# Optimization experiments

Hardware: AMD Instinct MI355X
Metric: run time of the kernel (lower is better)

Reference implementation:

```python
import jax, jax.numpy as jnp
import numpy as np

D_MODEL = 1024
N_HEADS = 16
D_HEAD = D_MODEL // N_HEADS
B, T = 4, 2048


def setup_inputs() -> dict:
    key = jax.random.key(0)
    k1, k2, k3 = jax.random.split(key, 3)
    x = jax.random.normal(k1, (B, T, D_MODEL), dtype=jnp.float32)
    # torch nn.Linear(d, 3d, bias=False): y = x @ W.T; here we store W.T directly.
    w_qkv = jax.random.normal(k2, (D_MODEL, 3 * D_MODEL), dtype=jnp.float32) * (1.0 / np.sqrt(D_MODEL))
    w_proj = jax.random.normal(k3, (D_MODEL, D_MODEL), dtype=jnp.float32) * (1.0 / np.sqrt(D_MODEL))
    return {"x": x, "w_qkv": w_qkv, "w_proj": w_proj}


def reference(x, w_qkv, w_proj):
    b, t, _ = x.shape
    qkv = x @ w_qkv  # [B, T, 3*D]
    q, k, v = jnp.split(qkv, 3, axis=-1)

    def split_heads(u):
        return u.reshape(b, t, N_HEADS, D_HEAD).transpose(0, 2, 1, 3)  # [B,H,T,Dh]

    q, k, v = split_heads(q), split_heads(k), split_heads(v)
    scale = 1.0 / np.sqrt(D_HEAD).astype(np.float32)
    scores = jnp.einsum('bhqd,bhkd->bhqk', q, k) * scale  # [B,H,T,T]
    attn = jax.nn.softmax(scores, axis=-1)
    out = jnp.einsum('bhqk,bhkd->bhqd', attn, v)  # [B,H,T,Dh]
    out = out.transpose(0, 2, 1, 3).reshape(b, t, D_MODEL)
    return out @ w_proj
```

## Files before the change

### kernel.cpp

```cpp
#include <hip/hip_runtime.h>
#include <hip/hip_bf16.h>
#include <stdint.h>

using bf16 = __bf16;
using bf16x8 = __attribute__((ext_vector_type(8))) __bf16;
using f32x4  = __attribute__((ext_vector_type(4))) float;
using f32x16 = __attribute__((ext_vector_type(16))) float;
using u32x4  = __attribute__((ext_vector_type(4))) uint32_t;

#define LOG2E 1.44269504088896340736f

constexpr int Tt = 2048;
constexpr int Dm = 1024;
constexpr int NH = 16;
constexpr int DH = 64;

__device__ inline void gll16(const void* g, void* l) {
  __builtin_amdgcn_global_load_lds((const __attribute__((address_space(1))) uint32_t*)g,
                                   (__attribute__((address_space(3))) uint32_t*)l, 16, 0, 0);
}

__device__ inline uint32_t cvtpk(float a, float b) {
  uint32_t r;
  asm("v_cvt_pk_bf16_f32 %0, %1, %2" : "=v"(r) : "v"(a), "v"(b));
  return r;
}
__device__ inline void pl32swap(uint32_t& a, uint32_t& b) {
  asm("v_permlane32_swap_b32 %0, %1" : "+v"(a), "+v"(b));
}
__device__ inline bf16x8 mkfrag(uint32_t w0, uint32_t w1, uint32_t w2, uint32_t w3) {
  u32x4 t; t[0] = w0; t[1] = w1; t[2] = w2; t[3] = w3;
  return __builtin_bit_cast(bf16x8, t);
}

__global__ void k_cvt_x(const float* __restrict__ x, bf16* __restrict__ xb) {
  size_t i = (size_t)blockIdx.x * blockDim.x + threadIdx.x;
  float4 v0 = ((const float4*)x)[i * 2];
  float4 v1 = ((const float4*)x)[i * 2 + 1];
  bf16x8 o;
  o[0]=(bf16)v0.x; o[1]=(bf16)v0.y; o[2]=(bf16)v0.z; o[3]=(bf16)v0.w;
  o[4]=(bf16)v1.x; o[5]=(bf16)v1.y; o[6]=(bf16)v1.z; o[7]=(bf16)v1.w;
  *(bf16x8*)(xb + i * 8) = o;
}

__global__ void k_tconv(const float* __restrict__ W, bf16* __restrict__ WT, int K, int N) {
  __shared__ float t[32][33];
  int n0 = blockIdx.x * 32, k0 = blockIdx.y * 32;
  int tx = threadIdx.x, ty = threadIdx.y;
  #pragma unroll
  for (int i = 0; i < 4; i++)
    t[ty + i * 8][tx] = W[(size_t)(k0 + ty + i * 8) * N + n0 + tx];
  __syncthreads();
  #pragma unroll
  for (int i = 0; i < 4; i++)
    WT[(size_t)(n0 + ty + i * 8) * K + k0 + tx] = (bf16)t[tx][ty + i * 8];
}

__global__ void k_tv(const bf16* __restrict__ v, bf16* __restrict__ vt) {
  __shared__ __attribute__((aligned(16))) bf16 t[64][72];
  int bh = blockIdx.y, t0 = blockIdx.x * 64;
  int tid = threadIdx.x;
  const bf16* src = v + ((size_t)bh * Tt + t0) * DH;
  #pragma unroll
  for (int rep = 0; rep < 2; rep++) {
    int c = tid + rep * 256;
    int tr = c >> 3, dc = (c & 7) * 8;
    *(bf16x8*)&t[tr][dc] = *(const bf16x8*)(src + tr * DH + dc);
  }
  __syncthreads();
  bf16* dst = vt + (size_t)bh * DH * Tt + t0;
  #pragma unroll
  for (int rep = 0; rep < 2; rep++) {
    int c = tid + rep * 256;
    int d = c >> 3, tc = (c & 7) * 8;
    bf16x8 o;
    #pragma unroll
    for (int j = 0; j < 8; j++) o[j] = t[tc + j][d];
    *(bf16x8*)(dst + (size_t)d * Tt + tc) = o;
  }
}

template <int EPI>
__global__ __launch_bounds__(256) void k_gemm(const bf16* __restrict__ A, const bf16* __restrict__ Bt,
                                              float* __restrict__ C,
                                              bf16* __restrict__ qb, bf16* __restrict__ kb, bf16* __restrict__ vb,
                                              int M, int N, int K) {
  __shared__ __attribute__((aligned(16))) bf16 As[128 * 32];
  __shared__ __attribute__((aligned(16))) bf16 Bs[128 * 32];
  char* Asb = (char*)As; char* Bsb = (char*)Bs;
  const int tid = threadIdx.x;
  const int m0 = blockIdx.y * 128, n0 = blockIdx.x * 128;
  const int wid = tid >> 6, lane = tid & 63, g = lane >> 4, lr = lane & 15;
  const int wr = wid >> 1, wc = wid & 1;
  f32x4 acc[4][4] = {};

  for (int k0 = 0; k0 < K; k0 += 32) {
    __syncthreads();
    #pragma unroll
    for (int rep = 0; rep < 2; rep++) {
      int c = tid + rep * 256;
      int row = c >> 2;
      int Lb = (c * 16) ^ (((c >> 3) & 3) << 4);
      int w = Lb & 63;
      gll16(A  + (size_t)(m0 + row) * K + k0 + (w >> 1), Asb + (wid * 64 + rep * 256) * 16);
      gll16(Bt + (size_t)(n0 + row) * K + k0 + (w >> 1), Bsb + (wid * 64 + rep * 256) * 16);
    }
    __syncthreads();
    bf16x8 a[4], b[4];
    #pragma unroll
    for (int m = 0; m < 4; m++) {
      int row = wr * 64 + m * 16 + lr;
      int addr = (row * 64 + g * 16) ^ (((row >> 1) & 3) << 4);
      a[m] = *(const bf16x8*)(Asb + addr);
    }
    #pragma unroll
    for (int n = 0; n < 4; n++) {
      int row = wc * 64 + n * 16 + lr;
      int addr = (row * 64 + g * 16) ^ (((row >> 1) & 3) << 4);
      b[n] = *(const bf16x8*)(Bsb + addr);
    }
    #pragma unroll
    for (int m = 0; m < 4; m++)
      #pragma unroll
      for (int n = 0; n < 4; n++)
        acc[m][n] = __builtin_amdgcn_mfma_f32_16x16x32_bf16(a[m], b[n], acc[m][n], 0, 0, 0);
  }

  #pragma unroll
  for (int m = 0; m < 4; m++) {
    #pragma unroll
    for (int n = 0; n < 4; n++) {
      int col = n0 + wc * 64 + n * 16 + lr;
      #pragma unroll
      for (int r = 0; r < 4; r++) {
        int row = m0 + wr * 64 + m * 16 + g * 4 + r;
        float val = acc[m][n][r];
        if (EPI == 0) {
          int bI = row >> 11, t = row & (Tt - 1);
          if (col < 1024) {
            int h = col >> 6, d = col & 63;
            qb[(((size_t)bI * NH + h) * Tt + t) * DH + d] = (bf16)(val * 0.18033688f);
          } else if (col < 2048) {
            int c2 = col - 1024; int h = c2 >> 6, d = c2 & 63;
            kb[(((size_t)bI * NH + h) * Tt + t) * DH + d] = (bf16)val;
          } else {
            int c2 = col - 2048; int h = c2 >> 6, d = c2 & 63;
            vb[(((size_t)bI * NH + h) * Tt + t) * DH + d] = (bf16)val;
          }
        } else {
          C[(size_t)row * N + col] = val;
        }
      }
    }
  }
}

__global__ __launch_bounds__(256) void k_attn(const bf16* __restrict__ qbuf, const bf16* __restrict__ kbuf,
                                              const bf16* __restrict__ vtbuf, bf16* __restrict__ ob) {
  __shared__ __attribute__((aligned(16))) bf16 Kt[64 * 64];
  __shared__ __attribute__((aligned(16))) bf16 Vt[64 * 64];
  __shared__ float Lred[4][32];
  char* KtB = (char*)Kt; char* VtB = (char*)Vt;

  const int bh = blockIdx.y;
  const int tid = threadIdx.x, wid = tid >> 6, lane = tid & 63;
  const int lo31 = lane & 31, hi = lane >> 5;
  const int qw = blockIdx.x * 128 + wid * 32;

  const bf16* qp = qbuf + (size_t)bh * Tt * DH;
  const char* kpB = (const char*)(kbuf + (size_t)bh * Tt * DH);
  const char* vpB = (const char*)(vtbuf + (size_t)bh * DH * Tt);

  bf16x8 qf[4];
  #pragma unroll
  for (int sl = 0; sl < 4; sl++)
    qf[sl] = *(const bf16x8*)(qp + (size_t)(qw + lo31) * DH + sl * 16 + hi * 8);

  f32x16 o0 = 0.f, o1 = 0.f;
  float lsum = 0.f;

  const int swz = (lo31 & 7) << 4;

  for (int kt = 0; kt < Tt; kt += 64) {
    __syncthreads();
    #pragma unroll
    for (int rep = 0; rep < 2; rep++) {
      int c = rep * 256 + wid * 64 + lane;
      int row = c >> 3, w = (c & 7) * 16;
      int sw = w ^ ((row & 7) << 4);
      gll16(kpB + (size_t)kt * 128 + row * 128 + sw, KtB + (rep * 256 + wid * 64) * 16);
      gll16(vpB + (size_t)row * (Tt * 2) + kt * 2 + sw, VtB + (rep * 256 + wid * 64) * 16);
    }
    __syncthreads();

    f32x16 s0 = 0.f, s1 = 0.f;
    #pragma unroll
    for (int sl = 0; sl < 4; sl++) {
      bf16x8 k0 = *(const bf16x8*)(KtB + lo31 * 128 + ((sl * 32 + hi * 16) ^ swz));
      bf16x8 k1 = *(const bf16x8*)(KtB + (32 + lo31) * 128 + ((sl * 32 + hi * 16) ^ swz));
      s0 = __builtin_amdgcn_mfma_f32_32x32x16_bf16(k0, qf[sl], s0, 0, 0, 0);
      s1 = __builtin_amdgcn_mfma_f32_32x32x16_bf16(k1, qf[sl], s1, 0, 0, 0);
    }

    bf16x8 pa[4];
    #pragma unroll
    for (int i = 0; i < 16; i++) { float p = __builtin_amdgcn_exp2f(s0[i]); s0[i] = p; lsum += p; }
    #pragma unroll
    for (int i = 0; i < 16; i++) { float p = __builtin_amdgcn_exp2f(s1[i]); s1[i] = p; lsum += p; }
    {
      uint32_t a0 = cvtpk(s0[0], s0[1]), b0 = cvtpk(s0[4], s0[5]);  pl32swap(a0, b0);
      uint32_t a1 = cvtpk(s0[2], s0[3]), b1 = cvtpk(s0[6], s0[7]);  pl32swap(a1, b1);
      pa[0] = mkfrag(a0, a1, b0, b1);
      uint32_t a2 = cvtpk(s0[8], s0[9]),  b2 = cvtpk(s0[12], s0[13]); pl32swap(a2, b2);
      uint32_t a3 = cvtpk(s0[10], s0[11]), b3 = cvtpk(s0[14], s0[15]); pl32swap(a3, b3);
      pa[1] = mkfrag(a2, a3, b2, b3);
      uint32_t c0 = cvtpk(s1[0], s1[1]), d0 = cvtpk(s1[4], s1[5]);  pl32swap(c0, d0);
      uint32_t c1 = cvtpk(s1[2], s1[3]), d1 = cvtpk(s1[6], s1[7]);  pl32swap(c1, d1);
      pa[2] = mkfrag(c0, c1, d0, d1);
      uint32_t c2 = cvtpk(s1[8], s1[9]),  d2 = cvtpk(s1[12], s1[13]); pl32swap(c2, d2);
      uint32_t c3 = cvtpk(s1[10], s1[11]), d3 = cvtpk(s1[14], s1[15]); pl32swap(c3, d3);
      pa[3] = mkfrag(c2, c3, d2, d3);
    }

    #pragma unroll
    for (int sl = 0; sl < 4; sl++) {
      bf16x8 v0 = *(const bf16x8*)(VtB + lo31 * 128 + ((sl * 32 + hi * 16) ^ swz));
      bf16x8 v1 = *(const bf16x8*)(VtB + (32 + lo31) * 128 + ((sl * 32 + hi * 16) ^ swz));
      o0 = __builtin_amdgcn_mfma_f32_32x32x16_bf16(pa[sl], v0, o0, 0, 0, 0);
      o1 = __builtin_amdgcn_mfma_f32_32x32x16_bf16(pa[sl], v1, o1, 0, 0, 0);
    }
  }

  lsum += __shfl_xor(lsum, 32);
  Lred[wid][lo31] = lsum;
  __syncthreads();

  int bI = bh >> 4, h = bh & 15;
  #pragma unroll
  for (int reg = 0; reg < 16; reg++) {
    int qr = (reg & 3) + 8 * (reg >> 2) + 4 * hi;
    float inv = 1.0f / Lred[wid][qr];
    size_t base = ((size_t)(bI * Tt + qw + qr)) * Dm + h * 64;
    ob[base + lo31]      = (bf16)(o0[reg] * inv);
    ob[base + 32 + lo31] = (bf16)(o1[reg] * inv);
  }
}

extern "C" void kernel_launch(void* const* d_in, const int* in_sizes, int n_in,
                              void* d_out, int out_size, void* d_ws, size_t ws_size,
                              hipStream_t stream) {
  const float* x     = (const float*)d_in[0];
  const float* wqkv  = (const float*)d_in[1];
  const float* wproj = (const float*)d_in[2];
  float* out = (float*)d_out;
  char* ws = (char*)d_ws;

  bf16* xb     = (bf16*)(ws);
  bf16* wqkvT  = (bf16*)(ws + 16777216);
  bf16* wprojT = (bf16*)(ws + 23068672);
  bf16* qb     = (bf16*)(ws + 25165824);
  bf16* kb     = (bf16*)(ws + 41943040);
  bf16* vb     = (bf16*)(ws + 58720256);
  bf16* attn   = (bf16*)(ws + 75497472);
  bf16* vt     = xb;

  k_cvt_x<<<4096, 256, 0, stream>>>(x, xb);
  k_tconv<<<dim3(96, 32), dim3(32, 8), 0, stream>>>(wqkv, wqkvT, 1024, 3072);
  k_tconv<<<dim3(32, 32), dim3(32, 8), 0, stream>>>(wproj, wprojT, 1024, 1024);
  k_gemm<0><<<dim3(24, 64), 256, 0, stream>>>(xb, wqkvT, nullptr, qb, kb, vb, 8192, 3072, 1024);
  k_tv<<<dim3(32, 64), 256, 0, stream>>>(vb, vt);
  k_attn<<<dim3(16, 64), 256, 0, stream>>>(qb, kb, vt, attn);
  k_gemm<1><<<dim3(8, 64), 256, 0, stream>>>(attn, wprojT, out, nullptr, nullptr, nullptr, 8192, 1024, 1024);
}
```

Baseline: 307.3 us.

## Double-buffer K/V tiles in attention and remap blocks for XCD locality

The attention kernel now keeps two LDS buffers for K and V and issues the next tile's global-to-LDS loads before computing on the current tile. This is meant to hide load latency and drops one barrier per iteration. Both GEMM and attention launches remap block ids so that consecutive work is grouped per XCD (id&7), which should improve L2 reuse of K/V and of weight tiles. MFMA sections are wrapped in s_setprio. The cost is doubled LDS use in attention, which may reduce occupancy.

```diff
diff --git a/kernel.cpp b/kernel.cpp
--- a/kernel.cpp
+++ b/kernel.cpp
@@ -89,7 +89,10 @@
   __shared__ __attribute__((aligned(16))) bf16 Bs[128 * 32];
   char* Asb = (char*)As; char* Bsb = (char*)Bs;
   const int tid = threadIdx.x;
-  const int m0 = blockIdx.y * 128, n0 = blockIdx.x * 128;
+  int id = blockIdx.y * gridDim.x + blockIdx.x;
+  int cpx = (gridDim.x * gridDim.y) >> 3;
+  id = (id & 7) * cpx + (id >> 3);
+  const int m0 = (id / gridDim.x) * 128, n0 = (id % gridDim.x) * 128;
   const int wid = tid >> 6, lane = tid & 63, g = lane >> 4, lr = lane & 15;
   const int wr = wid >> 1, wc = wid & 1;
   f32x4 acc[4][4] = {};
@@ -157,15 +160,18 @@
 
 __global__ __launch_bounds__(256) void k_attn(const bf16* __restrict__ qbuf, const bf16* __restrict__ kbuf,
                                               const bf16* __restrict__ vtbuf, bf16* __restrict__ ob) {
-  __shared__ __attribute__((aligned(16))) bf16 Kt[64 * 64];
-  __shared__ __attribute__((aligned(16))) bf16 Vt[64 * 64];
+  __shared__ __attribute__((aligned(16))) bf16 Kt[2][64 * 64];
+  __shared__ __attribute__((aligned(16))) bf16 Vt[2][64 * 64];
   __shared__ float Lred[4][32];
-  char* KtB = (char*)Kt; char* VtB = (char*)Vt;
-
-  const int bh = blockIdx.y;
+
+  int id = blockIdx.x;
+  id = (id & 7) * 128 + (id >> 3);
+  const int bh = id >> 4;
+  const int qblk = id & 15;
+
   const int tid = threadIdx.x, wid = tid >> 6, lane = tid & 63;
   const int lo31 = lane & 31, hi = lane >> 5;
-  const int qw = blockIdx.x * 128 + wid * 32;
+  const int qw = qblk * 128 + wid * 32;
 
   const bf16* qp = qbuf + (size_t)bh * Tt * DH;
   const char* kpB = (const char*)(kbuf + (size_t)bh * Tt * DH);
@@ -178,22 +184,31 @@
 
   f32x16 o0 = 0.f, o1 = 0.f;
   float lsum = 0.f;
-
   const int swz = (lo31 & 7) << 4;
 
-  for (int kt = 0; kt < Tt; kt += 64) {
-    __syncthreads();
+  auto STAGE = [&](int buf, int kt) {
+    char* KB = (char*)Kt[buf]; char* VB = (char*)Vt[buf];
     #pragma unroll
     for (int rep = 0; rep < 2; rep++) {
       int c = rep * 256 + wid * 64 + lane;
       int row = c >> 3, w = (c & 7) * 16;
       int sw = w ^ ((row & 7) << 4);
-      gll16(kpB + (size_t)kt * 128 + row * 128 + sw, KtB + (rep * 256 + wid * 64) * 16);
-      gll16(vpB + (size_t)row * (Tt * 2) + kt * 2 + sw, VtB + (rep * 256 + wid * 64) * 16);
-    }
-    __syncthreads();
+      gll16(kpB + (size_t)kt * 128 + row * 128 + sw, KB + (rep * 256 + wid * 64) * 16);
+      gll16(vpB + (size_t)row * (Tt * 2) + kt * 2 + sw, VB + (rep * 256 + wid * 64) * 16);
+    }
+  };
+
+  STAGE(0, 0);
+  __syncthreads();
+
+  for (int it = 0; it < Tt / 64; ++it) {
+    int cur = it & 1;
+    if (it + 1 < Tt / 64) STAGE(cur ^ 1, (it + 1) * 64);
+    char* KtB = (char*)Kt[cur];
+    char* VtB = (char*)Vt[cur];
 
     f32x16 s0 = 0.f, s1 = 0.f;
+    __builtin_amdgcn_s_setprio(1);
     #pragma unroll
     for (int sl = 0; sl < 4; sl++) {
       bf16x8 k0 = *(const bf16x8*)(KtB + lo31 * 128 + ((sl * 32 + hi * 16) ^ swz));
@@ -201,6 +216,7 @@
       s0 = __builtin_amdgcn_mfma_f32_32x32x16_bf16(k0, qf[sl], s0, 0, 0, 0);
       s1 = __builtin_amdgcn_mfma_f32_32x32x16_bf16(k1, qf[sl], s1, 0, 0, 0);
     }
+    __builtin_amdgcn_s_setprio(0);
 
     bf16x8 pa[4];
     #pragma unroll
@@ -222,6 +238,7 @@
       pa[3] = mkfrag(c2, c3, d2, d3);
     }
 
+    __builtin_amdgcn_s_setprio(1);
     #pragma unroll
     for (int sl = 0; sl < 4; sl++) {
       bf16x8 v0 = *(const bf16x8*)(VtB + lo31 * 128 + ((sl * 32 + hi * 16) ^ swz));
@@ -229,6 +246,9 @@
       o0 = __builtin_amdgcn_mfma_f32_32x32x16_bf16(pa[sl], v0, o0, 0, 0, 0);
       o1 = __builtin_amdgcn_mfma_f32_32x32x16_bf16(pa[sl], v1, o1, 0, 0, 0);
     }
+    __builtin_amdgcn_s_setprio(0);
+
+    __syncthreads();
   }
 
   lsum += __shfl_xor(lsum, 32);
@@ -269,6 +289,6 @@
   k_tconv<<<dim3(32, 32), dim3(32, 8), 0, stream>>>(wproj, wprojT, 1024, 1024);
   k_gemm<0><<<dim3(24, 64), 256, 0, stream>>>(xb, wqkvT, nullptr, qb, kb, vb, 8192, 3072, 1024);
   k_tv<<<dim3(32, 64), 256, 0, stream>>>(vb, vt);
-  k_attn<<<dim3(16, 64), 256, 0, stream>>>(qb, kb, vt, attn);
+  k_attn<<<1024, 256, 0, stream>>>(qb, kb, vt, attn);
   k_gemm<1><<<dim3(8, 64), 256, 0, stream>>>(attn, wprojT, out, nullptr, nullptr, nullptr, 8192, 1024, 1024);
 }
```

Measured after the change: 301.5 us. Within noise of the previous version (-1.9%).
